# Performance work log

Hardware: AMD Instinct MI355X
Metric: run time of the kernel (lower is better)

The kernel has to match this reference:

```python
import jax, jax.numpy as jnp
import numpy as np
import math

B, S, E, H, F, V, L = 2, 2048, 1024, 16, 4096, 32000, 2
D = E // H
START = 1
EPS = 1e-6


def setup_inputs() -> dict:
    key = jax.random.key(0)
    ks = jax.random.split(key, 16)
    k_emb = 1.0 / math.sqrt(V)
    std = 0.02
    inp = {
        "tokens": jax.random.randint(ks[0], (B, S), 0, V),
        "word_embed": jax.random.normal(ks[1], (V, E), jnp.float32) * k_emb,
        "pos_embed": jax.random.normal(ks[2], (S, E), jnp.float32) * k_emb,
        "unembed_b": jnp.zeros((V,), jnp.float32),
        "kqv_w": jax.random.normal(ks[3], (L, 3 * E, E), jnp.float32) * std,
        "wo_w": jax.random.normal(ks[4], (L, E, E), jnp.float32) * std,
        "up_w": jax.random.normal(ks[5], (L, F, E), jnp.float32) * std,
        "up_b": jnp.zeros((L, F), jnp.float32),
        "down_w": jax.random.normal(ks[6], (L, E, F), jnp.float32) * std,
        "down_b": jnp.zeros((L, E), jnp.float32),
        "ln1_s": jnp.ones((L, E), jnp.float32),
        "ln1_b": jnp.zeros((L, E), jnp.float32),
        "ln2_s": jnp.ones((L, E), jnp.float32),
        "ln2_b": jnp.zeros((L, E), jnp.float32),
    }
    return inp


def _layer_norm(x, scale, bias):
    m = jnp.mean(x, axis=-1, keepdims=True)
    v = jnp.var(x, axis=-1, keepdims=True)  # biased, matches torch LayerNorm
    return (x - m) / jnp.sqrt(v + EPS) * scale + bias


def _causal_block_mask(tokens):
    # block-diagonal segments split at START tokens, plus causal triu
    is_start = tokens == START
    seg = jnp.cumsum(is_start, axis=1)  # [B,S]
    block = seg[:, :, None] != seg[:, None, :]  # [B,S,S]
    triu = jnp.triu(jnp.ones((S, S), bool), k=1)
    return triu[None, :, :] | block  # [B,S,S], True = masked


def _resetting_positions(tokens):
    is_start = tokens == START
    is_start = is_start.at[:, 0].set(True)
    pos = jnp.arange(S)
    start_pos = jnp.where(is_start, pos[None, :], 0)
    last_start = jax.lax.cummax(start_pos, axis=1)
    return pos[None, :] - last_start  # [B,S]


def reference(tokens, word_embed, pos_embed, unembed_b, kqv_w, wo_w,
              up_w, up_b, down_w, down_b, ln1_s, ln1_b, ln2_s, ln2_b):
    mask = _causal_block_mask(tokens)[:, None, :, :]  # [B,1,S,S]
    rel_pos = _resetting_positions(tokens)
    x = word_embed[tokens] + pos_embed[rel_pos]  # [B,S,E]
    scale = 1.0 / math.sqrt(D)

    for l in range(L):
        # attention
        qkv = (x @ kqv_w[l].T).reshape(B, S, 3, H, D)
        k, q, v = qkv[:, :, 0], qkv[:, :, 1], qkv[:, :, 2]  # [B,S,H,D]
        attn = jnp.einsum('bqhd,bkhd->bhqk', q, k) * scale
        attn = jnp.where(mask, -jnp.inf, attn)
        attn = jax.nn.softmax(attn, axis=-1)
        out = jnp.einsum('bhqk,bkhd->bqhd', attn, v).reshape(B, S, E)
        out = out @ wo_w[l].T
        x = _layer_norm(out + x, ln1_s[l], ln1_b[l])
        # FFN
        h = jax.nn.relu(x @ up_w[l].T + up_b[l])
        h = h @ down_w[l].T + down_b[l]
        x = _layer_norm(h + x, ln2_s[l], ln2_b[l])

    # weight-tied unembed
    logits = x @ word_embed.T + unembed_b  # [B,S,V]
    return logits
```

## Files before the change

### kernel.cpp

```cpp
#include <hip/hip_runtime.h>
#include <hip/hip_bf16.h>

#define BB 2
#define SS 2048
#define EE 1024
#define HH 16
#define DD 64
#define FF 4096
#define VV 32000
#define LL 2
#define BS (BB*SS)

#define NEG_HUGE (-3.402823466e+38f)

typedef __attribute__((ext_vector_type(4)))  float  f32x4;
typedef __attribute__((ext_vector_type(16))) float  f32x16;
typedef __attribute__((ext_vector_type(8)))  __bf16 bf16x8;
typedef __attribute__((ext_vector_type(4)))  __bf16 bf16x4;

__device__ inline bf16x8 to_bf8(float4 a, float4 b) {
  bf16x8 r;
  r[0] = (__bf16)a.x; r[1] = (__bf16)a.y; r[2] = (__bf16)a.z; r[3] = (__bf16)a.w;
  r[4] = (__bf16)b.x; r[5] = (__bf16)b.y; r[6] = (__bf16)b.z; r[7] = (__bf16)b.w;
  return r;
}

typedef const unsigned int __attribute__((address_space(1)))* gptr_t;
typedef unsigned int __attribute__((address_space(3)))* lptr_t;
__device__ inline void gload16(const void* g, void* l) {
  __builtin_amdgcn_global_load_lds((gptr_t)g, (lptr_t)l, 16, 0, 0);
}

__global__ __launch_bounds__(1024) void lastart_scan(
    const int* __restrict__ tokens, int* __restrict__ ls) {
  __shared__ int buf[SS];
  const int b = blockIdx.x, t = threadIdx.x;
#pragma unroll
  for (int j = 0; j < 2; ++j) {
    int i = t + j * 1024;
    buf[i] = (i > 0 && tokens[b*SS + i] == 1) ? i : 0;
  }
  __syncthreads();
  for (int off = 1; off < SS; off <<= 1) {
    int i0 = t, i1 = t + 1024;
    int v0 = (i0 >= off) ? max(buf[i0], buf[i0 - off]) : buf[i0];
    int v1 = (i1 >= off) ? max(buf[i1], buf[i1 - off]) : buf[i1];
    __syncthreads();
    buf[i0] = v0; buf[i1] = v1;
    __syncthreads();
  }
#pragma unroll
  for (int j = 0; j < 2; ++j) {
    int i = t + j * 1024;
    ls[b*SS + i] = buf[i];
  }
}

__global__ __launch_bounds__(256) void embed_kernel(
    const int* __restrict__ tokens, const int* __restrict__ ls,
    const float* __restrict__ we, const float* __restrict__ pe,
    float* __restrict__ x, __bf16* __restrict__ xb) {
  int row = blockIdx.x;
  int s = row & (SS - 1);
  int tok = tokens[row];
  int rp = s - ls[row];
  const float4* w4 = (const float4*)(we + (size_t)tok * EE);
  const float4* p4 = (const float4*)(pe + (size_t)rp * EE);
  float4 a = w4[threadIdx.x];
  float4 b = p4[threadIdx.x];
  float4 o; o.x = a.x + b.x; o.y = a.y + b.y; o.z = a.z + b.z; o.w = a.w + b.w;
  ((float4*)(x + (size_t)row * EE))[threadIdx.x] = o;
  bf16x4 ob4;
  ob4[0] = (__bf16)o.x; ob4[1] = (__bf16)o.y; ob4[2] = (__bf16)o.z; ob4[3] = (__bf16)o.w;
  *(bf16x4*)(xb + (size_t)row * EE + threadIdx.x * 4) = ob4;
}

__global__ __launch_bounds__(256) void cvt_bf16_kernel(
    const float* __restrict__ src, __bf16* __restrict__ dst, int n) {
  int i = (blockIdx.x * 256 + threadIdx.x) * 8;
  if (i + 8 > n) return;
  float4 a = *(const float4*)(src + i);
  float4 b = *(const float4*)(src + i + 4);
  *(bf16x8*)(dst + i) = to_bf8(a, b);
}

template<int T, int BM>
__device__ inline void stage2(const __bf16* __restrict__ Ab,
                              const __bf16* __restrict__ Wb,
                              __bf16* la, __bf16* lb, int K, int k0, int t) {
  const int col8 = (t & 3) ^ ((t >> 3) & 3);
  const int cofs = k0 + col8 * 8;
  const int wbase = (t >> 6) * 512;
#pragma unroll
  for (int p = 0; p < (BM * 32) / (T * 8); ++p) {
    const int row = p * (T >> 2) + (t >> 2);
    gload16(Ab + (size_t)row * K + cofs, la + p * T * 8 + wbase);
    gload16(Wb + (size_t)row * K + cofs, lb + p * T * 8 + wbase);
  }
}

template<int RW, int WM, int WN, bool BIAS, bool RELU, bool OUTBF16>
__global__ __launch_bounds__(WM*WN*64, 2) void gemm_deep(
    const __bf16* __restrict__ A, const __bf16* __restrict__ W,
    const float* __restrict__ bias, void* __restrict__ Cv,
    int N, int K, int nbx) {
  constexpr int T  = WM * WN * 64;
  constexpr int BM = WM * RW * 16;
  __shared__ __bf16 lds[4][2][BM * 32];
  const int t = threadIdx.x, l = t & 63, w = t >> 6;
  const int nwg = gridDim.x, orig = blockIdx.x;
  const int q = nwg >> 3, r = nwg & 7, xcd = orig & 7, pos = orig >> 3;
  const int wgid = (xcd < r ? xcd*(q+1) : r*(q+1) + (xcd-r)*q) + pos;
  const int m0 = (wgid % nbx) * BM, n0 = (wgid / nbx) * BM;
  const int wm = w / WN, wn = w % WN;
  const int fr = l & 15, c8 = l >> 4;
  const int slot = (c8 ^ ((fr >> 1) & 3)) * 8;

  const __bf16* Abase = A + (size_t)m0 * K;
  const __bf16* Wbase = W + (size_t)n0 * K;

  f32x4 acc[RW][4] = {};

  const int nk = K >> 5;
  stage2<T,BM>(Abase, Wbase, &lds[0][0][0], &lds[0][1][0], K, 0,  t);
  stage2<T,BM>(Abase, Wbase, &lds[1][0][0], &lds[1][1][0], K, 32, t);
  stage2<T,BM>(Abase, Wbase, &lds[2][0][0], &lds[2][1][0], K, 64, t);

  for (int kt = 0; kt < nk; ++kt) {
    const int cur = kt & 3;
    if (kt + 3 < nk) {
      const int nb = (kt + 3) & 3;
      stage2<T,BM>(Abase, Wbase, &lds[nb][0][0], &lds[nb][1][0], K, (kt+3)*32, t);
      asm volatile("s_waitcnt vmcnt(8)" ::: "memory");
    } else if (kt + 2 < nk) {
      asm volatile("s_waitcnt vmcnt(8)" ::: "memory");
    } else if (kt + 1 < nk) {
      asm volatile("s_waitcnt vmcnt(4)" ::: "memory");
    } else {
      asm volatile("s_waitcnt vmcnt(0)" ::: "memory");
    }
    __builtin_amdgcn_s_barrier();
    __builtin_amdgcn_sched_barrier(0);
    const __bf16* La = &lds[cur][0][0];
    const __bf16* Lb = &lds[cur][1][0];
    bf16x8 bfr[4];
#pragma unroll
    for (int j = 0; j < 4; ++j)
      bfr[j] = *(const bf16x8*)&Lb[(wn*64 + j*16 + fr) * 32 + slot];
    __builtin_amdgcn_s_setprio(1);
#pragma unroll
    for (int i = 0; i < RW; ++i) {
      bf16x8 af = *(const bf16x8*)&La[(wm*(RW*16) + i*16 + fr) * 32 + slot];
#pragma unroll
      for (int j = 0; j < 4; ++j)
        acc[i][j] = __builtin_amdgcn_mfma_f32_16x16x32_bf16(af, bfr[j], acc[i][j], 0, 0, 0);
    }
    __builtin_amdgcn_s_setprio(0);
    __builtin_amdgcn_sched_barrier(0);
    __builtin_amdgcn_s_barrier();
    __builtin_amdgcn_sched_barrier(0);
  }

  const int orow = m0 + wm*(RW*16) + c8 * 4;
  const int ocol = n0 + wn*64 + fr;
#pragma unroll
  for (int i = 0; i < RW; ++i)
#pragma unroll
    for (int j = 0; j < 4; ++j) {
      const int col = ocol + j * 16;
      const float bv = BIAS ? bias[col] : 0.0f;
#pragma unroll
      for (int rr = 0; rr < 4; ++rr) {
        float v = acc[i][j][rr] + bv;
        if (RELU) v = fmaxf(v, 0.0f);
        if (OUTBF16)
          ((__bf16*)Cv)[(size_t)(orow + i*16 + rr) * N + col] = (__bf16)v;
        else
          ((float*)Cv)[(size_t)(orow + i*16 + rr) * N + col] = v;
      }
    }
}

template<bool WBF16, bool BIAS, bool RELU, bool OUTBF16>
__global__ __launch_bounds__(256) void gemm_fast(
    const __bf16* __restrict__ A, const void* __restrict__ Wv,
    const float* __restrict__ bias, void* __restrict__ Cv, int N, int K) {
  __shared__ __bf16 As[128][32];
  __shared__ __bf16 Bs[128][32];
  const int t = threadIdx.x;
  const int m0 = blockIdx.x * 128, n0 = blockIdx.y * 128;
  const int l = t & 63, w = t >> 6;
  const int wm = (w >> 1) * 64, wn = (w & 1) * 64;
  const int fr = l & 15, fk = (l >> 4) * 8;
  const int crow = l >> 2, ccol = (l & 3) * 8;
  const int wrow = t >> 1, wcol = (t & 1) * 16;

  const __bf16* Wb = (const __bf16*)Wv;
  const float*  Wf = (const float*)Wv;

  f32x4 acc[4][4] = {};

  for (int k0 = 0; k0 < K; k0 += 32) {
    float4 wf0, wf1, wf2, wf3;
    if (!WBF16) {
      const float* wp = Wf + (size_t)(n0 + wrow) * K + k0 + wcol;
      wf0 = *(const float4*)(wp);
      wf1 = *(const float4*)(wp + 4);
      wf2 = *(const float4*)(wp + 8);
      wf3 = *(const float4*)(wp + 12);
    }
    __syncthreads();
#pragma unroll
    for (int i = 0; i < 2; ++i) {
      const int c = 2 * w + i;
      gload16(A + (size_t)(m0 + c*16 + crow) * K + k0 + ccol, (__bf16*)As + c*512);
      if (WBF16)
        gload16(Wb + (size_t)(n0 + c*16 + crow) * K + k0 + ccol, (__bf16*)Bs + c*512);
    }
    if (!WBF16) {
      *(bf16x8*)&Bs[wrow][wcol]     = to_bf8(wf0, wf1);
      *(bf16x8*)&Bs[wrow][wcol + 8] = to_bf8(wf2, wf3);
    }
    __syncthreads();
    bf16x8 af[4], bf[4];
#pragma unroll
    for (int i = 0; i < 4; ++i) af[i] = *(const bf16x8*)&As[wm + i*16 + fr][fk];
#pragma unroll
    for (int j = 0; j < 4; ++j) bf[j] = *(const bf16x8*)&Bs[wn + j*16 + fr][fk];
#pragma unroll
    for (int i = 0; i < 4; ++i)
#pragma unroll
      for (int j = 0; j < 4; ++j)
        acc[i][j] = __builtin_amdgcn_mfma_f32_16x16x32_bf16(af[i], bf[j], acc[i][j], 0, 0, 0);
  }

  const int orow = m0 + wm + (l >> 4) * 4;
  const int ocol = n0 + wn + fr;
#pragma unroll
  for (int i = 0; i < 4; ++i)
#pragma unroll
    for (int j = 0; j < 4; ++j) {
      const int col = ocol + j * 16;
      const float bv = BIAS ? bias[col] : 0.0f;
#pragma unroll
      for (int r = 0; r < 4; ++r) {
        float v = acc[i][j][r] + bv;
        if (RELU) v = fmaxf(v, 0.0f);
        if (OUTBF16)
          ((__bf16*)Cv)[(size_t)(orow + i*16 + r) * N + col] = (__bf16)v;
        else
          ((float*)Cv)[(size_t)(orow + i*16 + r) * N + col] = v;
      }
    }
}

__global__ __launch_bounds__(256) void ln_res_kernel(
    const float* __restrict__ y, float* __restrict__ x, __bf16* __restrict__ xb,
    const float* __restrict__ sc, const float* __restrict__ bs) {
  __shared__ float red[8];
  int row = blockIdx.x, t = threadIdx.x;
  const float4* y4 = (const float4*)(y + (size_t)row * EE);
  float4* x4 = (float4*)(x + (size_t)row * EE);
  float4 a = y4[t], c = x4[t];
  float v0 = a.x + c.x, v1 = a.y + c.y, v2 = a.z + c.z, v3 = a.w + c.w;
  float s = v0 + v1 + v2 + v3;
  float q = v0*v0 + v1*v1 + v2*v2 + v3*v3;
#pragma unroll
  for (int off = 32; off; off >>= 1) {
    s += __shfl_xor(s, off);
    q += __shfl_xor(q, off);
  }
  int w = t >> 6;
  if ((t & 63) == 0) { red[w] = s; red[4 + w] = q; }
  __syncthreads();
  s = red[0] + red[1] + red[2] + red[3];
  q = red[4] + red[5] + red[6] + red[7];
  float mean = s * (1.0f / EE);
  float var  = q * (1.0f / EE) - mean * mean;
  float r = 1.0f / sqrtf(var + 1e-6f);
  float4 ss = ((const float4*)sc)[t];
  float4 bb = ((const float4*)bs)[t];
  float4 o;
  o.x = (v0 - mean) * r * ss.x + bb.x;
  o.y = (v1 - mean) * r * ss.y + bb.y;
  o.z = (v2 - mean) * r * ss.z + bb.z;
  o.w = (v3 - mean) * r * ss.w + bb.w;
  x4[t] = o;
  bf16x4 ob4;
  ob4[0] = (__bf16)o.x; ob4[1] = (__bf16)o.y; ob4[2] = (__bf16)o.z; ob4[3] = (__bf16)o.w;
  *(bf16x4*)(xb + (size_t)row * EE + t * 4) = ob4;
}

__global__ __launch_bounds__(256) void attn_mfma(
    const __bf16* __restrict__ qkv, const int* __restrict__ ls,
    __bf16* __restrict__ out) {
  const int qt = 15 - blockIdx.x;
  const int h = blockIdx.y, b = blockIdx.z;
  __shared__ f32x4 lds4[2304];
  char* lds = (char*)lds4;
  __bf16* Ks = (__bf16*)lds;
  __bf16* Vs = (__bf16*)(lds + 9216);
  __shared__ int redmin[4];
  const int t = threadIdx.x, w = t >> 6, l = t & 63;
  __bf16* Pq = (__bf16*)(lds + 18432 + w * 4608);
  const int r = l & 31, hi = l >> 5;
  const int qb = qt * 128, qw = qb + w * 32, qg = qw + r;
  const int Lq = ls[b*SS + qg];

  {
    int mn = Lq;
#pragma unroll
    for (int off = 1; off < 64; off <<= 1) mn = min(mn, __shfl_xor(mn, off));
    if (l == 0) redmin[w] = mn;
  }

  bf16x8 qf[4];
  {
    const __bf16* qrow = qkv + (size_t)(b*SS + qg) * 3*EE + EE + h*DD + 8*hi;
#pragma unroll
    for (int ds = 0; ds < 4; ++ds) qf[ds] = *(const bf16x8*)(qrow + 16*ds);
  }
  __syncthreads();
  const int ktmin = min(min(redmin[0], redmin[1]), min(redmin[2], redmin[3])) >> 6;
  const int ktmax = 2*qt + 1;

  f32x16 oacc[2] = {};
  float m_r = NEG_HUGE, lsum = 0.0f;

  for (int kt = ktmin; kt <= ktmax; ++kt) {
    __syncthreads();
    {
      const int kr = t >> 2, c0 = (t & 3) * 16;
      const __bf16* kg = qkv + (size_t)(b*SS + kt*64 + kr) * 3*EE + h*DD + c0;
      const __bf16* vg = kg + 2*EE;
      bf16x8 k0 = *(const bf16x8*)kg;
      bf16x8 k1 = *(const bf16x8*)(kg + 8);
      bf16x8 v0 = *(const bf16x8*)vg;
      bf16x8 v1 = *(const bf16x8*)(vg + 8);
      *(bf16x8*)&Ks[kr*72 + c0]     = k0;
      *(bf16x8*)&Ks[kr*72 + c0 + 8] = k1;
      const int vc = (kr + 8*(t & 3)) & 63;
#pragma unroll
      for (int j = 0; j < 8; ++j) {
        Vs[(c0 + j)*72 + vc]     = v0[j];
        Vs[(c0 + 8 + j)*72 + vc] = v1[j];
      }
    }
    __syncthreads();

    bool act0 = (kt*64)      <= (qw + 31);
    bool act1 = (kt*64 + 32) <= (qw + 31);
    if (!act0) continue;

    f32x16 st[2];
    st[0] = (f32x16){};
    st[1] = (f32x16){};
#pragma unroll
    for (int ds = 0; ds < 4; ++ds) {
      bf16x8 kf = *(const bf16x8*)&Ks[(r)*72 + 16*ds + 8*hi];
      st[0] = __builtin_amdgcn_mfma_f32_32x32x16_bf16(kf, qf[ds], st[0], 0, 0, 0);
    }
    if (act1) {
#pragma unroll
      for (int ds = 0; ds < 4; ++ds) {
        bf16x8 kf = *(const bf16x8*)&Ks[(32 + r)*72 + 16*ds + 8*hi];
        st[1] = __builtin_amdgcn_mfma_f32_32x32x16_bf16(kf, qf[ds], st[1], 0, 0, 0);
      }
    }

    float tmax = NEG_HUGE;
#pragma unroll
    for (int kt2 = 0; kt2 < 2; ++kt2) {
#pragma unroll
      for (int reg = 0; reg < 16; ++reg) {
        const int key = kt*64 + 32*kt2 + (reg & 3) + 8*(reg >> 2) + 4*hi;
        float s = (kt2 == 0 || act1) ? st[kt2][reg] * 0.125f : NEG_HUGE;
        const bool valid = (key >= Lq) && (key <= qg);
        s = valid ? s : NEG_HUGE;
        st[kt2][reg] = s;
        tmax = fmaxf(tmax, s);
      }
    }
    tmax = fmaxf(tmax, __shfl_xor(tmax, 32));
    const float m_new = fmaxf(m_r, tmax);
    const float alpha = __expf(m_r - m_new);
    m_r = m_new;

    float psum = 0.0f;
#pragma unroll
    for (int kt2 = 0; kt2 < 2; ++kt2) {
#pragma unroll
      for (int g2 = 0; g2 < 4; ++g2) {
        bf16x4 pk;
#pragma unroll
        for (int j = 0; j < 4; ++j) {
          float p = __expf(st[kt2][g2*4 + j] - m_new);
          psum += p;
          pk[j] = (__bf16)p;
        }
        *(bf16x4*)&Pq[r*72 + 32*kt2 + 8*g2 + 4*hi] = pk;
      }
    }
    psum += __shfl_xor(psum, 32);
    lsum = lsum * alpha + psum;
    oacc[0] *= alpha;
    oacc[1] *= alpha;

#pragma unroll
    for (int ks = 0; ks < 4; ++ks) {
      if (kt*64 + 16*ks > qw + 31) continue;
      bf16x8 pf = *(const bf16x8*)&Pq[r*72 + 16*ks + 8*hi];
#pragma unroll
      for (int mt = 0; mt < 2; ++mt) {
        const int d = 32*mt + r;
        const int vcol = (16*ks + 8*hi + 8*((d >> 4) & 3)) & 63;
        bf16x8 vf = *(const bf16x8*)&Vs[d*72 + vcol];
        oacc[mt] = __builtin_amdgcn_mfma_f32_32x32x16_bf16(vf, pf, oacc[mt], 0, 0, 0);
      }
    }
  }

  __syncthreads();
  float* Ot = (float*)(lds + w * 8448);
  const float rinv = 1.0f / lsum;
#pragma unroll
  for (int mt = 0; mt < 2; ++mt)
#pragma unroll
    for (int reg = 0; reg < 16; ++reg) {
      const int d = 32*mt + (reg & 3) + 8*(reg >> 2) + 4*hi;
      Ot[d*33 + r] = oacc[mt][reg] * rinv;
    }
  __syncthreads();
  const int qr0 = l >> 4, dc = (l & 15) * 4;
#pragma unroll
  for (int it = 0; it < 8; ++it) {
    const int qr = qr0 + 4*it;
    bf16x4 ov;
    ov[0] = (__bf16)Ot[(dc+0)*33 + qr];
    ov[1] = (__bf16)Ot[(dc+1)*33 + qr];
    ov[2] = (__bf16)Ot[(dc+2)*33 + qr];
    ov[3] = (__bf16)Ot[(dc+3)*33 + qr];
    *(bf16x4*)(out + (size_t)(b*SS + qw + qr) * EE + h*DD + dc) = ov;
  }
}

extern "C" void kernel_launch(void* const* d_in, const int* in_sizes, int n_in,
                              void* d_out, int out_size, void* d_ws, size_t ws_size,
                              hipStream_t stream) {
  const int*   tokens     = (const int*)  d_in[0];
  const float* word_embed = (const float*)d_in[1];
  const float* pos_embed  = (const float*)d_in[2];
  const float* unembed_b  = (const float*)d_in[3];
  const float* kqv_w      = (const float*)d_in[4];
  const float* wo_w       = (const float*)d_in[5];
  const float* up_w       = (const float*)d_in[6];
  const float* up_b       = (const float*)d_in[7];
  const float* down_w     = (const float*)d_in[8];
  const float* down_b     = (const float*)d_in[9];
  const float* ln1_s      = (const float*)d_in[10];
  const float* ln1_b      = (const float*)d_in[11];
  const float* ln2_s      = (const float*)d_in[12];
  const float* ln2_b      = (const float*)d_in[13];
  float* logits = (float*)d_out;

  char* ob = (char*)d_out;
  __bf16* qkv  = (__bf16*)ob;
  __bf16* t0   = (__bf16*)(ob +  24ull*1024*1024);
  __bf16* hbuf = (__bf16*)(ob +  32ull*1024*1024);
  float*  ybuf = (float*) (ob +  64ull*1024*1024);
  __bf16* wcvt = (__bf16*)(ob +  80ull*1024*1024);
  float*  x    = (float*) (ob + 131ull*1024*1024);
  __bf16* kqvb  = wcvt;
  __bf16* wob   = kqvb + (size_t)LL*3*EE*EE;
  __bf16* upb   = wob  + (size_t)LL*EE*EE;
  __bf16* downb = upb  + (size_t)LL*FF*EE;
  int*    ls   = (int*)d_ws;
  __bf16* xb   = (__bf16*)((char*)d_ws + 65536);
  __bf16* webf = (__bf16*)((char*)d_ws + 65536 + 8ull*1024*1024);
  const bool bigws = ws_size >= (size_t)(65536 + 8ull*1024*1024 + (size_t)VV*EE*2);

  lastart_scan<<<BB, 1024, 0, stream>>>(tokens, ls);
  embed_kernel<<<BS, 256, 0, stream>>>(tokens, ls, word_embed, pos_embed, x, xb);

  cvt_bf16_kernel<<<LL*3*EE*EE/2048, 256, 0, stream>>>(kqv_w,  kqvb,  LL*3*EE*EE);
  cvt_bf16_kernel<<<LL*EE*EE/2048,   256, 0, stream>>>(wo_w,   wob,   LL*EE*EE);
  cvt_bf16_kernel<<<LL*FF*EE/2048,   256, 0, stream>>>(up_w,   upb,   LL*FF*EE);
  cvt_bf16_kernel<<<LL*EE*FF/2048,   256, 0, stream>>>(down_w, downb, LL*EE*FF);
  if (bigws)
    cvt_bf16_kernel<<<VV*EE/2048, 256, 0, stream>>>(word_embed, webf, VV*EE);

  for (int l = 0; l < LL; ++l) {
    gemm_deep<8,2,4,false,false,true><<<(BS/256)*(3*EE/256), 512, 0, stream>>>(
        xb, kqvb + (size_t)l*3*EE*EE, nullptr, qkv, 3*EE, EE, BS/256);
    attn_mfma<<<dim3(16, HH, BB), 256, 0, stream>>>(qkv, ls, t0);
    gemm_deep<4,2,2,false,false,false><<<(BS/128)*(EE/128), 256, 0, stream>>>(
        t0, wob + (size_t)l*EE*EE, nullptr, ybuf, EE, EE, BS/128);
    ln_res_kernel<<<BS, 256, 0, stream>>>(ybuf, x, xb, ln1_s + l*EE, ln1_b + l*EE);
    gemm_deep<8,2,4,true,true,true><<<(BS/256)*(FF/256), 512, 0, stream>>>(
        xb, upb + (size_t)l*FF*EE, up_b + (size_t)l*FF, hbuf, FF, EE, BS/256);
    gemm_deep<4,2,2,true,false,false><<<(BS/128)*(EE/128), 256, 0, stream>>>(
        hbuf, downb + (size_t)l*EE*FF, down_b + (size_t)l*EE, ybuf, EE, FF, BS/128);
    ln_res_kernel<<<BS, 256, 0, stream>>>(ybuf, x, xb, ln2_s + l*EE, ln2_b + l*EE);
  }

  if (bigws)
    gemm_deep<8,2,4,true,false,false><<<(BS/256)*(VV/256), 512, 0, stream>>>(
        xb, webf, unembed_b, logits, VV, EE, BS/256);
  else
    gemm_fast<false,true,false,false><<<dim3(BS/128, VV/128), 256, 0, stream>>>(
        xb, word_embed, unembed_b, logits, VV, EE);
}
```

Baseline: 1.011 ms.

## Add 8-phase pipelined 256x256 bf16 GEMM kernel with interleaved half-tile staging

Introduces gemm_8ph, a 256x256-tile MFMA GEMM that splits each K=64 step into half-tiles and interleaves global-to-LDS loads of the next stages with four MFMA phases. It uses explicit vmcnt waits, barriers, setprio and XCD-aware workgroup remapping. It replaces gemm_deep for the QKV, up-projection and unembed GEMMs. The aim is to hide memory latency behind MFMA work, at the cost of many more barriers and fragile hand-tuned wait counts.

```diff
diff --git a/kernel.cpp b/kernel.cpp
--- a/kernel.cpp
+++ b/kernel.cpp
@@ -82,6 +82,159 @@
   float4 a = *(const float4*)(src + i);
   float4 b = *(const float4*)(src + i + 4);
   *(bf16x8*)(dst + i) = to_bf8(a, b);
+}
+
+__device__ inline void stage_half(const __bf16* __restrict__ base,
+                                  __bf16* region, int K, int kofs, int t) {
+  const int col8 = (t & 3) ^ ((t >> 3) & 3);
+  const int csrc = kofs + col8 * 8;
+  const int wbase = (t >> 6) * 512;
+#pragma unroll
+  for (int p = 0; p < 2; ++p)
+    gload16(base + (size_t)(p * 128 + (t >> 2)) * K + csrc, region + p * 4096 + wbase);
+}
+
+#define SWZ(row) ((c8 ^ (((row) >> 1) & 3)) * 8)
+
+template<bool BIAS, bool RELU, bool OUTBF16>
+__global__ __launch_bounds__(512, 2) void gemm_8ph(
+    const __bf16* __restrict__ A, const __bf16* __restrict__ W,
+    const float* __restrict__ bias, void* __restrict__ Cv,
+    int N, int K, int nbx) {
+  __shared__ __bf16 lds[2][2][2][8192];
+  const int t = threadIdx.x, l = t & 63, w = t >> 6;
+  const int nwg = gridDim.x, orig = blockIdx.x;
+  const int q = nwg >> 3, r = nwg & 7, xcd = orig & 7, pos = orig >> 3;
+  const int wgid = (xcd < r ? xcd*(q+1) : r*(q+1) + (xcd-r)*q) + pos;
+  const int m0 = (wgid % nbx) * 256, n0 = (wgid / nbx) * 256;
+  const int wm = w >> 2, wn = w & 3;
+  const int fr = l & 15, c8 = l >> 4;
+
+  const __bf16* Ab = A + (size_t)m0 * K;
+  const __bf16* Wb = W + (size_t)n0 * K;
+
+  f32x4 acc[8][4] = {};
+  const int nk = K >> 6;
+
+  stage_half(Ab, &lds[0][0][0][0], K, 0,  t);
+  stage_half(Wb, &lds[0][1][0][0], K, 0,  t);
+  stage_half(Ab, &lds[0][0][1][0], K, 32, t);
+  stage_half(Wb, &lds[0][1][1][0], K, 32, t);
+  stage_half(Ab, &lds[1][0][0][0], K, 64, t);
+  stage_half(Wb, &lds[1][1][0][0], K, 64, t);
+  asm volatile("s_waitcnt vmcnt(4)" ::: "memory");
+  __builtin_amdgcn_s_barrier();
+  __builtin_amdgcn_sched_barrier(0);
+
+  for (int kt = 0; kt < nk; ++kt) {
+    const int c = kt & 1;
+    bf16x8 afr[4], bfr[4];
+#pragma unroll
+    for (int j = 0; j < 4; ++j) {
+      const int row = wn*64 + j*16 + fr;
+      bfr[j] = *(const bf16x8*)&lds[c][1][0][row*32 + SWZ(row)];
+    }
+#pragma unroll
+    for (int i = 0; i < 4; ++i) {
+      const int row = wm*128 + i*16 + fr;
+      afr[i] = *(const bf16x8*)&lds[c][0][0][row*32 + SWZ(row)];
+    }
+    if (kt + 1 < nk) stage_half(Ab, &lds[c^1][0][1][0], K, (kt+1)*64 + 32, t);
+    __builtin_amdgcn_s_barrier();
+    __builtin_amdgcn_sched_barrier(0);
+    __builtin_amdgcn_s_setprio(1);
+#pragma unroll
+    for (int i = 0; i < 4; ++i)
+#pragma unroll
+      for (int j = 0; j < 4; ++j)
+        acc[i][j] = __builtin_amdgcn_mfma_f32_16x16x32_bf16(afr[i], bfr[j], acc[i][j], 0, 0, 0);
+    __builtin_amdgcn_s_setprio(0);
+    __builtin_amdgcn_sched_barrier(0);
+    __builtin_amdgcn_s_barrier();
+    __builtin_amdgcn_sched_barrier(0);
+#pragma unroll
+    for (int i = 0; i < 4; ++i) {
+      const int row = wm*128 + (i+4)*16 + fr;
+      afr[i] = *(const bf16x8*)&lds[c][0][0][row*32 + SWZ(row)];
+    }
+    if (kt + 1 < nk) stage_half(Wb, &lds[c^1][1][1][0], K, (kt+1)*64 + 32, t);
+    __builtin_amdgcn_s_barrier();
+    __builtin_amdgcn_sched_barrier(0);
+    __builtin_amdgcn_s_setprio(1);
+#pragma unroll
+    for (int i = 0; i < 4; ++i)
+#pragma unroll
+      for (int j = 0; j < 4; ++j)
+        acc[i+4][j] = __builtin_amdgcn_mfma_f32_16x16x32_bf16(afr[i], bfr[j], acc[i+4][j], 0, 0, 0);
+    __builtin_amdgcn_s_setprio(0);
+    __builtin_amdgcn_sched_barrier(0);
+    if (kt < nk - 1) { asm volatile("s_waitcnt vmcnt(8)" ::: "memory"); }
+    else             { asm volatile("s_waitcnt vmcnt(0)" ::: "memory"); }
+    __builtin_amdgcn_s_barrier();
+    __builtin_amdgcn_sched_barrier(0);
+#pragma unroll
+    for (int j = 0; j < 4; ++j) {
+      const int row = wn*64 + j*16 + fr;
+      bfr[j] = *(const bf16x8*)&lds[c][1][1][row*32 + SWZ(row)];
+    }
+#pragma unroll
+    for (int i = 0; i < 4; ++i) {
+      const int row = wm*128 + i*16 + fr;
+      afr[i] = *(const bf16x8*)&lds[c][0][1][row*32 + SWZ(row)];
+    }
+    if (kt + 2 < nk) stage_half(Ab, &lds[c][0][0][0], K, (kt+2)*64, t);
+    __builtin_amdgcn_s_barrier();
+    __builtin_amdgcn_sched_barrier(0);
+    __builtin_amdgcn_s_setprio(1);
+#pragma unroll
+    for (int i = 0; i < 4; ++i)
+#pragma unroll
+      for (int j = 0; j < 4; ++j)
+        acc[i][j] = __builtin_amdgcn_mfma_f32_16x16x32_bf16(afr[i], bfr[j], acc[i][j], 0, 0, 0);
+    __builtin_amdgcn_s_setprio(0);
+    __builtin_amdgcn_sched_barrier(0);
+    __builtin_amdgcn_s_barrier();
+    __builtin_amdgcn_sched_barrier(0);
+#pragma unroll
+    for (int i = 0; i < 4; ++i) {
+      const int row = wm*128 + (i+4)*16 + fr;
+      afr[i] = *(const bf16x8*)&lds[c][0][1][row*32 + SWZ(row)];
+    }
+    if (kt + 2 < nk) stage_half(Wb, &lds[c][1][0][0], K, (kt+2)*64, t);
+    __builtin_amdgcn_s_barrier();
+    __builtin_amdgcn_sched_barrier(0);
+    __builtin_amdgcn_s_setprio(1);
+#pragma unroll
+    for (int i = 0; i < 4; ++i)
+#pragma unroll
+      for (int j = 0; j < 4; ++j)
+        acc[i+4][j] = __builtin_amdgcn_mfma_f32_16x16x32_bf16(afr[i], bfr[j], acc[i+4][j], 0, 0, 0);
+    __builtin_amdgcn_s_setprio(0);
+    __builtin_amdgcn_sched_barrier(0);
+    if (kt < nk - 2)       { asm volatile("s_waitcnt vmcnt(8)" ::: "memory"); }
+    else if (kt == nk - 2) { asm volatile("s_waitcnt vmcnt(4)" ::: "memory"); }
+    __builtin_amdgcn_s_barrier();
+    __builtin_amdgcn_sched_barrier(0);
+  }
+
+  const int orow = m0 + wm*128 + c8 * 4;
+  const int ocol = n0 + wn*64 + fr;
+#pragma unroll
+  for (int i = 0; i < 8; ++i)
+#pragma unroll
+    for (int j = 0; j < 4; ++j) {
+      const int col = ocol + j * 16;
+      const float bv = BIAS ? bias[col] : 0.0f;
+#pragma unroll
+      for (int rr = 0; rr < 4; ++rr) {
+        float v = acc[i][j][rr] + bv;
+        if (RELU) v = fmaxf(v, 0.0f);
+        if (OUTBF16)
+          ((__bf16*)Cv)[(size_t)(orow + i*16 + rr) * N + col] = (__bf16)v;
+        else
+          ((float*)Cv)[(size_t)(orow + i*16 + rr) * N + col] = v;
+      }
+    }
 }
 
 template<int T, int BM>
@@ -490,13 +643,13 @@
     cvt_bf16_kernel<<<VV*EE/2048, 256, 0, stream>>>(word_embed, webf, VV*EE);
 
   for (int l = 0; l < LL; ++l) {
-    gemm_deep<8,2,4,false,false,true><<<(BS/256)*(3*EE/256), 512, 0, stream>>>(
+    gemm_8ph<false,false,true><<<(BS/256)*(3*EE/256), 512, 0, stream>>>(
         xb, kqvb + (size_t)l*3*EE*EE, nullptr, qkv, 3*EE, EE, BS/256);
     attn_mfma<<<dim3(16, HH, BB), 256, 0, stream>>>(qkv, ls, t0);
     gemm_deep<4,2,2,false,false,false><<<(BS/128)*(EE/128), 256, 0, stream>>>(
         t0, wob + (size_t)l*EE*EE, nullptr, ybuf, EE, EE, BS/128);
     ln_res_kernel<<<BS, 256, 0, stream>>>(ybuf, x, xb, ln1_s + l*EE, ln1_b + l*EE);
-    gemm_deep<8,2,4,true,true,true><<<(BS/256)*(FF/256), 512, 0, stream>>>(
+    gemm_8ph<true,true,true><<<(BS/256)*(FF/256), 512, 0, stream>>>(
         xb, upb + (size_t)l*FF*EE, up_b + (size_t)l*FF, hbuf, FF, EE, BS/256);
     gemm_deep<4,2,2,true,false,false><<<(BS/128)*(EE/128), 256, 0, stream>>>(
         hbuf, downb + (size_t)l*EE*FF, down_b + (size_t)l*EE, ybuf, EE, FF, BS/128);
@@ -504,7 +657,7 @@
   }
 
   if (bigws)
-    gemm_deep<8,2,4,true,false,false><<<(BS/256)*(VV/256), 512, 0, stream>>>(
+    gemm_8ph<true,false,false><<<(BS/256)*(VV/256), 512, 0, stream>>>(
         xb, webf, unembed_b, logits, VV, EE, BS/256);
   else
     gemm_fast<false,true,false,false><<<dim3(BS/128, VV/128), 256, 0, stream>>>(
```

After: 983.0 us. 2.8% less time.
